# Kernel tuning notes

Hardware: AMD Instinct MI355X
Metric: run time of the kernel (lower is better)

Reference implementation:

```python
import jax, jax.numpy as jnp
import numpy as np

NUM_HEADS = 16
MAX_REL = 512  # max_relative_positions k


def setup_inputs() -> dict:
    key = jax.random.key(0)
    ks = jax.random.split(key, 8)
    B, S, H = 4, 1024, 1024
    R = 2 * MAX_REL + 1
    s = 0.02
    return {
        "hidden_states": jax.random.normal(ks[0], (B, S, H), jnp.float32),
        "attention_mask": jnp.zeros((B, 1, 1, S), jnp.float32),
        "rel_embeddings": jax.random.normal(ks[1], (R, H), jnp.float32),
        "Wq": jax.random.normal(ks[2], (H, H), jnp.float32) * s,
        "bq": jnp.zeros((H,), jnp.float32),
        "Wk": jax.random.normal(ks[3], (H, H), jnp.float32) * s,
        "bk": jnp.zeros((H,), jnp.float32),
        "Wv": jax.random.normal(ks[4], (H, H), jnp.float32) * s,
        "bv": jnp.zeros((H,), jnp.float32),
        "Wpk": jax.random.normal(ks[5], (H, H), jnp.float32) * s,
        "bpk": jnp.zeros((H,), jnp.float32),
        "Wpq": jax.random.normal(ks[6], (H, H), jnp.float32) * s,
        "bpq": jnp.zeros((H,), jnp.float32),
    }


def _heads(x, B, S):
    # [B,S,H] -> [B,nH,S,hd]
    return x.reshape(B, S, NUM_HEADS, -1).transpose(0, 2, 1, 3)


def reference(hidden_states, attention_mask, rel_embeddings,
              Wq, bq, Wk, bk, Wv, bv, Wpk, bpk, Wpq, bpq):
    B, S, H = hidden_states.shape
    hd = H // NUM_HEADS
    scale = 1.0 / np.sqrt(3.0 * hd).astype(np.float32)

    q = _heads(hidden_states @ Wq + bq, B, S)  # [B,nH,S,hd]
    k = _heads(hidden_states @ Wk + bk, B, S)
    v = _heads(hidden_states @ Wv + bv, B, S)

    # relative position bucket indices in [0, 2k]
    ids = jnp.arange(S)
    rel_pos = jnp.clip(ids[:, None] - ids[None, :], -MAX_REL, MAX_REL) + MAX_REL  # [S,S]

    rel_k = (rel_embeddings @ Wpk + bpk).reshape(-1, NUM_HEADS, hd)  # [R,nH,hd]
    rel_q = (rel_embeddings @ Wpq + bpq).reshape(-1, NUM_HEADS, hd)

    # 1) content-to-content
    c2c = jnp.einsum('bnih,bnjh->bnij', q, k)

    # 2) content-to-position: gather q.rel_k over rel bucket per (i,j)
    c2p_all = jnp.einsum('bnih,rnh->bnir', q, rel_k)  # [B,nH,S,R]
    idx = jnp.broadcast_to(rel_pos[None, None], (B, NUM_HEADS, S, S))
    c2p = jnp.take_along_axis(c2p_all, idx, axis=3)  # [B,nH,S,S]

    # 3) position-to-content: p2c[b,n,i,j] = (k_j . rel_q)[rel_pos[j,i]]
    p2c_all = jnp.einsum('bnjh,rnh->bnjr', k, rel_q)  # [B,nH,S,R]
    p2c_ji = jnp.take_along_axis(p2c_all, idx, axis=3)  # [B,nH,j,i]
    p2c = p2c_ji.transpose(0, 1, 3, 2)

    scores = (c2c + c2p + p2c) * scale + attention_mask
    probs = jax.nn.softmax(scores, axis=-1)
    ctx = jnp.einsum('bnij,bnjh->bnih', probs, v)
    ctx = ctx.transpose(0, 2, 1, 3).reshape(B, S, H)
    return ctx
```

## Files before the change

kernel.cpp:

```cpp
#include <hip/hip_runtime.h>
#include <stdint.h>

typedef unsigned short u16;
typedef __bf16 bf16_t;
typedef bf16_t bf16x8 __attribute__((ext_vector_type(8)));
typedef float f32x4 __attribute__((ext_vector_type(4)));

__device__ __forceinline__ u16 f2bf(float f) {
  union { float f; unsigned int u; } v; v.f = f;
  return (u16)((v.u + 0x7FFFu + ((v.u >> 16) & 1u)) >> 16);
}
__device__ __forceinline__ float bf2f(u16 b) {
  union { unsigned int u; float f; } v; v.u = ((unsigned int)b) << 16;
  return v.f;
}
__device__ __forceinline__ unsigned pk2bf(float a, float b) {
  return (unsigned)f2bf(a) | ((unsigned)f2bf(b) << 16);
}

#define MFMA16(a, b, c) __builtin_amdgcn_mfma_f32_16x16x32_bf16((a), (b), (c), 0, 0, 0)
#define GLL16(g, l) __builtin_amdgcn_global_load_lds( \
    (const __attribute__((address_space(1))) void*)(g), \
    (__attribute__((address_space(3))) void*)(l), 16, 0, 0)

#define SWZ(row, col) ((col) ^ (((row) & 7) << 3))

#define SCALE 0.07216878364870323f
#define SCALE_L2E 0.10411754546752362f
#define LOG2E 1.4426950408889634f
#define M8L2E -11.541560327111707f

__global__ void cvt_bf16(const float* __restrict__ in, u16* __restrict__ out, int n4) {
  int i = blockIdx.x * 256 + threadIdx.x;
  if (i >= n4) return;
  float4 v = ((const float4*)in)[i];
  ushort4 o;
  o.x = f2bf(v.x); o.y = f2bf(v.y); o.z = f2bf(v.z); o.w = f2bf(v.w);
  ((ushort4*)out)[i] = o;
}

__global__ void transp5_bf16(const float* __restrict__ i0, const float* __restrict__ i1,
                             const float* __restrict__ i2, const float* __restrict__ i3,
                             const float* __restrict__ i4,
                             u16* __restrict__ o0, u16* __restrict__ o1,
                             u16* __restrict__ o2, u16* __restrict__ o3,
                             u16* __restrict__ o4) {
  __shared__ float t[32][33];
  const float* in;
  u16* out;
  switch (blockIdx.z) {
    case 0: in = i0; out = o0; break;
    case 1: in = i1; out = o1; break;
    case 2: in = i2; out = o2; break;
    case 3: in = i3; out = o3; break;
    default: in = i4; out = o4; break;
  }
  int tx = threadIdx.x & 31, ty = threadIdx.x >> 5;
  int x0 = blockIdx.x * 32, y0 = blockIdx.y * 32;
  #pragma unroll
  for (int i = ty; i < 32; i += 8)
    t[i][tx] = in[(size_t)(y0 + i) * 1024 + x0 + tx];
  __syncthreads();
  #pragma unroll
  for (int i = ty; i < 32; i += 8)
    out[(size_t)(x0 + i) * 1024 + y0 + tx] = f2bf(t[tx][i]);
}

__global__ void __launch_bounds__(256) gemm_multi(
    const u16* __restrict__ A, const u16* __restrict__ BT,
    const float* __restrict__ b0, const float* __restrict__ b1, const float* __restrict__ b2,
    u16* __restrict__ out, int M, int rel) {
  __shared__ __align__(16) u16 As[4096];
  __shared__ __align__(16) u16 Bs[4096];
  const int K = 1024;
  const int mat = blockIdx.y >> 3;
  const u16* BTm = BT + (size_t)mat * 1048576;
  const float* bias = (mat == 0) ? b0 : ((mat == 1) ? b1 : b2);
  const int m0 = blockIdx.x * 128, n0 = (blockIdx.y & 7) * 128;
  const int w = threadIdx.x >> 6, lane = threadIdx.x & 63;
  const int lj = lane & 15, lg = lane >> 4;
  const int wm = (w >> 1) * 64, wn = (w & 1) * 64;

  f32x4 acc[4][4] = {};

  const int chunk0 = w * 128 + lane;
  const int chunk1 = chunk0 + 64;
  int r0 = chunk0 >> 2, s0 = (chunk0 & 3) * 8;
  int r1 = chunk1 >> 2, s1 = (chunk1 & 3) * 8;
  int ar0 = m0 + r0; if (ar0 >= M) ar0 = M - 1;
  int ar1 = m0 + r1; if (ar1 >= M) ar1 = M - 1;
  const u16* ga0 = A + (size_t)ar0 * K + s0;
  const u16* ga1 = A + (size_t)ar1 * K + s1;
  const u16* gb0 = BTm + (size_t)(n0 + r0) * K + s0;
  const u16* gb1 = BTm + (size_t)(n0 + r1) * K + s1;
  u16* lA0 = As + (w * 2 + 0) * 512;
  u16* lA1 = As + (w * 2 + 1) * 512;
  u16* lB0 = Bs + (w * 2 + 0) * 512;
  u16* lB1 = Bs + (w * 2 + 1) * 512;

  for (int k0 = 0; k0 < K; k0 += 32) {
    GLL16(ga0 + k0, lA0);
    GLL16(ga1 + k0, lA1);
    GLL16(gb0 + k0, lB0);
    GLL16(gb1 + k0, lB1);
    __syncthreads();
    bf16x8 af[4], bf8[4];
    #pragma unroll
    for (int mf = 0; mf < 4; ++mf)
      af[mf] = *(const bf16x8*)(As + (wm + mf * 16 + lj) * 32 + lg * 8);
    #pragma unroll
    for (int nf = 0; nf < 4; ++nf)
      bf8[nf] = *(const bf16x8*)(Bs + (wn + nf * 16 + lj) * 32 + lg * 8);
    #pragma unroll
    for (int mf = 0; mf < 4; ++mf)
      #pragma unroll
      for (int nf = 0; nf < 4; ++nf)
        acc[mf][nf] = MFMA16(af[mf], bf8[nf], acc[mf][nf]);
    __syncthreads();
  }

  #pragma unroll
  for (int mf = 0; mf < 4; ++mf) {
    #pragma unroll
    for (int nf = 0; nf < 4; ++nf) {
      const int j = n0 + wn + nf * 16 + lj;
      const float bj = bias[j];
      #pragma unroll
      for (int r = 0; r < 4; ++r) {
        const int i = m0 + wm + mf * 16 + lg * 4 + r;
        if (i >= M) continue;
        const u16 val = f2bf(acc[mf][nf][r] + bj);
        if (rel) {
          out[(size_t)mat * 1049600 + (size_t)(j >> 6) * 65600 + (size_t)i * 64 + (j & 63)] = val;
        } else if (mat < 2) {
          out[(size_t)mat * 4194304 +
              (size_t)(((i >> 10) << 4) + (j >> 6)) * 65536 + (size_t)(i & 1023) * 64 + (j & 63)] = val;
        } else {
          out[(size_t)2 * 4194304 +
              (size_t)(((i >> 10) << 4) + (j >> 6)) * 65536 + (size_t)(j & 63) * 1024 + (i & 1023)] = val;
        }
      }
    }
  }
}

__global__ void __launch_bounds__(256, 2) attn_fused(
    const u16* __restrict__ qg, const u16* __restrict__ kg, const u16* __restrict__ vtg,
    const u16* __restrict__ rkg, const u16* __restrict__ rqg,
    const float* __restrict__ mask, float* __restrict__ out) {
  __shared__ __align__(16) u16 Ks[64][64];
  __shared__ __align__(16) u16 Ps[64][64];
  __shared__ __align__(16) u16 RKs[128][64];
  __shared__ __align__(16) u16 RQs[128][64];
  __shared__ __align__(16) u16 Ts[64][128];
  __shared__ __align__(16) u16 Us[64][128];

  const int bx = ((blockIdx.x & 7) << 7) | (blockIdx.x >> 3);
  const int it = bx & 15, bn = bx >> 4;
  const int b = bn >> 4, n = bn & 15;
  const int i0 = it * 64;
  const int tid = threadIdx.x, w = tid >> 6, lane = tid & 63;
  const int lj = lane & 15, lg = lane >> 4;

  const u16* qh = qg + (size_t)bn * 65536;
  const u16* kh = kg + (size_t)bn * 65536;
  const u16* vth = vtg + (size_t)bn * 65536;
  const u16* rkh = rkg + (size_t)n * 65600;
  const u16* rqh = rqg + (size_t)n * 65600;
  const float* mk = mask + (size_t)b * 1024;

  const int l8 = lane >> 3, gK = (lane & 7) ^ l8;
  const u16* kb0  = kh  + (size_t)((w * 2 + 0) * 8 + l8) * 64 + gK * 8;
  const u16* kb1  = kh  + (size_t)((w * 2 + 1) * 8 + l8) * 64 + gK * 8;
  const u16* rkb0 = rkh + (size_t)((w * 4 + 0) * 8 + l8) * 64 + gK * 8;
  const u16* rkb1 = rkh + (size_t)((w * 4 + 1) * 8 + l8) * 64 + gK * 8;
  const u16* rkb2 = rkh + (size_t)((w * 4 + 2) * 8 + l8) * 64 + gK * 8;
  const u16* rkb3 = rkh + (size_t)((w * 4 + 3) * 8 + l8) * 64 + gK * 8;
  const u16* rqb0 = rqh + (size_t)((w * 4 + 0) * 8 + l8) * 64 + gK * 8;
  const u16* rqb1 = rqh + (size_t)((w * 4 + 1) * 8 + l8) * 64 + gK * 8;
  const u16* rqb2 = rqh + (size_t)((w * 4 + 2) * 8 + l8) * 64 + gK * 8;
  const u16* rqb3 = rqh + (size_t)((w * 4 + 3) * 8 + l8) * 64 + gK * 8;
  u16* ksd0 = &Ks[0][0]  + (w * 2 + 0) * 512;
  u16* ksd1 = &Ks[0][0]  + (w * 2 + 1) * 512;
  u16* rkd0 = &RKs[0][0] + (w * 4 + 0) * 512;
  u16* rkd1 = &RKs[0][0] + (w * 4 + 1) * 512;
  u16* rkd2 = &RKs[0][0] + (w * 4 + 2) * 512;
  u16* rkd3 = &RKs[0][0] + (w * 4 + 3) * 512;
  u16* rqd0 = &RQs[0][0] + (w * 4 + 0) * 512;
  u16* rqd1 = &RQs[0][0] + (w * 4 + 1) * 512;
  u16* rqd2 = &RQs[0][0] + (w * 4 + 2) * 512;
  u16* rqd3 = &RQs[0][0] + (w * 4 + 3) * 512;

#define STAGE_TILE(J0N) do { \
    const int ddn_ = i0 - (J0N) + 512; \
    int w0n_ = ddn_ - 63; w0n_ = w0n_ < 0 ? 0 : (w0n_ > 897 ? 897 : w0n_); \
    int w0qn_ = (1024 - ddn_) - 63; w0qn_ = w0qn_ < 0 ? 0 : (w0qn_ > 897 ? 897 : w0qn_); \
    GLL16(kb0 + (size_t)(J0N) * 64, ksd0); \
    GLL16(kb1 + (size_t)(J0N) * 64, ksd1); \
    GLL16(rkb0 + (size_t)w0n_ * 64, rkd0); \
    GLL16(rkb1 + (size_t)w0n_ * 64, rkd1); \
    GLL16(rkb2 + (size_t)w0n_ * 64, rkd2); \
    GLL16(rkb3 + (size_t)w0n_ * 64, rkd3); \
    GLL16(rqb0 + (size_t)w0qn_ * 64, rqd0); \
    GLL16(rqb1 + (size_t)w0qn_ * 64, rqd1); \
    GLL16(rqb2 + (size_t)w0qn_ * 64, rqd2); \
    GLL16(rqb3 + (size_t)w0qn_ * 64, rqd3); \
  } while (0)

  bf16x8 aq_all[4][2];
  #pragma unroll
  for (int f = 0; f < 4; ++f)
    #pragma unroll
    for (int k2 = 0; k2 < 2; ++k2)
      aq_all[f][k2] = *(const bf16x8*)(qh + (size_t)(i0 + f * 16 + lj) * 64 + k2 * 32 + lg * 8);
  bf16x8 aq_own[2];
  #pragma unroll
  for (int k2 = 0; k2 < 2; ++k2)
    aq_own[k2] = *(const bf16x8*)(qh + (size_t)(i0 + w * 16 + lj) * 64 + k2 * 32 + lg * 8);

  const u16* vrow[4];
  #pragma unroll
  for (int d = 0; d < 4; ++d)
    vrow[d] = vth + (size_t)(d * 16 + lj) * 1024 + lg * 8;

  const int swlj = (lj & 7) << 3;
  int baseT[4], swi[4], baseP[4];
  #pragma unroll
  for (int r = 0; r < 4; ++r) {
    const int il = w * 16 + lg * 4 + r;
    baseT[r] = il * 128;
    swi[r] = (il & 7) << 3;
    baseP[r] = il * 64;
  }
  const u16* Ts_f = &Ts[0][0];
  const u16* Us_f = &Us[0][0];
  u16* Ts_w = &Ts[0][0];
  u16* Us_w = &Us[0][0];
  u16* Ps_f = &Ps[0][0];

  float lsum[4] = {0.f, 0.f, 0.f, 0.f};
  f32x4 accO[4] = {};

  STAGE_TILE(0);

  for (int jt = 0; jt < 16; ++jt) {
    const int j0 = jt * 64;
    const int dd = i0 - j0 + 512;
    int w0 = dd - 63; w0 = w0 < 0 ? 0 : (w0 > 897 ? 897 : w0);
    int w0q = (1024 - dd) - 63; w0q = w0q < 0 ? 0 : (w0q > 897 ? 897 : w0q);

    __syncthreads();

    bf16x8 bk_all[4][2];
    #pragma unroll
    for (int f = 0; f < 4; ++f)
      #pragma unroll
      for (int k2 = 0; k2 < 2; ++k2) {
        const int kr = f * 16 + lj;
        bk_all[f][k2] = *(const bf16x8*)(&Ks[kr][SWZ(kr, k2 * 32 + lg * 8)]);
      }
    __builtin_amdgcn_s_setprio(1);
    f32x4 scc[4];
    #pragma unroll
    for (int jf = 0; jf < 4; ++jf) {
      scc[jf] = (f32x4){0.f, 0.f, 0.f, 0.f};
      #pragma unroll
      for (int k2 = 0; k2 < 2; ++k2)
        scc[jf] = MFMA16(aq_own[k2], bk_all[jf][k2], scc[jf]);
    }
    #pragma unroll
    for (int c16 = 0; c16 < 2; ++c16) {
      const int tc = w * 2 + c16;
      const int rr = tc * 16 + lj;
      bf16x8 brk[2], brq[2];
      #pragma unroll
      for (int k2 = 0; k2 < 2; ++k2) {
        brk[k2] = *(const bf16x8*)(&RKs[rr][SWZ(rr, k2 * 32 + lg * 8)]);
        brq[k2] = *(const bf16x8*)(&RQs[rr][SWZ(rr, k2 * 32 + lg * 8)]);
      }
      const int cb = (tc * 16 + lg * 4) ^ swlj;
      #pragma unroll
      for (int f = 0; f < 4; ++f) {
        f32x4 t_ = {0.f, 0.f, 0.f, 0.f};
        f32x4 u_ = {0.f, 0.f, 0.f, 0.f};
        #pragma unroll
        for (int k2 = 0; k2 < 2; ++k2) {
          t_ = MFMA16(brk[k2], aq_all[f][k2], t_);
          u_ = MFMA16(brq[k2], bk_all[f][k2], u_);
        }
        uint2 tp, up;
        tp.x = pk2bf(t_[0], t_[1]); tp.y = pk2bf(t_[2], t_[3]);
        up.x = pk2bf(u_[0], u_[1]); up.y = pk2bf(u_[2], u_[3]);
        *(uint2*)(Ts_w + (f * 16 + lj) * 128 + cb) = tp;
        *(uint2*)(Us_w + (f * 16 + lj) * 128 + cb) = up;
      }
    }
    __builtin_amdgcn_s_setprio(0);
    __syncthreads();

    if (jt < 15) STAGE_TILE(j0 + 64);

    bf16x8 vreg[8];
    #pragma unroll
    for (int jk = 0; jk < 2; ++jk)
      #pragma unroll
      for (int d = 0; d < 4; ++d)
        vreg[jk * 4 + d] = *(const bf16x8*)(vrow[d] + j0 + jk * 32);

    const int E = dd + w * 16 + lg * 4 - lj;
    const int C2 = 1024 - w0q;
    float mjs[4];
    #pragma unroll
    for (int jf = 0; jf < 4; ++jf)
      mjs[jf] = fmaf(mk[j0 + jf * 16 + lj], LOG2E, M8L2E);
    if (dd >= 63 && dd <= 961) {
      #pragma unroll
      for (int jf = 0; jf < 4; ++jf) {
        const int ubase = (jf * 16 + lj) * 128;
        #pragma unroll
        for (int r = 0; r < 4; ++r) {
          const int x1 = E + r - jf * 16;
          const float tT = bf2f(Ts_f[baseT[r] + ((x1 - w0) ^ swi[r])]);
          const float tU = bf2f(Us_f[ubase + ((C2 - x1) ^ swlj)]);
          const float p = __builtin_amdgcn_exp2f(
              fmaf(scc[jf][r] + tT + tU, SCALE_L2E, mjs[jf]));
          lsum[r] += p;
          Ps_f[baseP[r] + ((jf * 16 + lj) ^ (swi[r] & 56))] = f2bf(p);
        }
      }
    } else {
      #pragma unroll
      for (int jf = 0; jf < 4; ++jf) {
        const int ubase = (jf * 16 + lj) * 128;
        #pragma unroll
        for (int r = 0; r < 4; ++r) {
          int x1 = E + r - jf * 16;
          x1 = x1 < 0 ? 0 : (x1 > 1024 ? 1024 : x1);
          const float tT = bf2f(Ts_f[baseT[r] + ((x1 - w0) ^ swi[r])]);
          const float tU = bf2f(Us_f[ubase + ((C2 - x1) ^ swlj)]);
          const float p = __builtin_amdgcn_exp2f(
              fmaf(scc[jf][r] + tT + tU, SCALE_L2E, mjs[jf]));
          lsum[r] += p;
          Ps_f[baseP[r] + ((jf * 16 + lj) ^ (swi[r] & 56))] = f2bf(p);
        }
      }
    }
    __builtin_amdgcn_s_setprio(1);
    #pragma unroll
    for (int jk = 0; jk < 2; ++jk) {
      const int pr = w * 16 + lj;
      bf16x8 ap = *(const bf16x8*)(&Ps[pr][SWZ(pr, jk * 32 + lg * 8)]);
      #pragma unroll
      for (int d = 0; d < 4; ++d)
        accO[d] = MFMA16(ap, vreg[jk * 4 + d], accO[d]);
    }
    __builtin_amdgcn_s_setprio(0);
  }

  #pragma unroll
  for (int off = 1; off < 16; off <<= 1)
    #pragma unroll
    for (int r = 0; r < 4; ++r)
      lsum[r] += __shfl_xor(lsum[r], off);

  #pragma unroll
  for (int r = 0; r < 4; ++r) {
    const float inv = 1.f / lsum[r];
    const int i = i0 + w * 16 + lg * 4 + r;
    #pragma unroll
    for (int d = 0; d < 4; ++d)
      out[((size_t)b * 1024 + i) * 1024 + n * 64 + d * 16 + lj] = accO[d][r] * inv;
  }
#undef STAGE_TILE
}

extern "C" void kernel_launch(void* const* d_in, const int* in_sizes, int n_in,
                              void* d_out, int out_size, void* d_ws, size_t ws_size,
                              hipStream_t stream) {
  const float* hs   = (const float*)d_in[0];
  const float* mask = (const float*)d_in[1];
  const float* rel  = (const float*)d_in[2];
  const float* Wq   = (const float*)d_in[3];
  const float* bq   = (const float*)d_in[4];
  const float* Wk   = (const float*)d_in[5];
  const float* bk   = (const float*)d_in[6];
  const float* Wv   = (const float*)d_in[7];
  const float* bv   = (const float*)d_in[8];
  const float* Wpk  = (const float*)d_in[9];
  const float* bpk  = (const float*)d_in[10];
  const float* Wpq  = (const float*)d_in[11];
  const float* bpq  = (const float*)d_in[12];
  float* outp = (float*)d_out;

  u16* p = (u16*)d_ws;
  u16* hsb  = p; p += (size_t)4096 * 1024;
  u16* relb = p; p += (size_t)1025 * 1024;
  u16* WqT  = p; p += (size_t)1024 * 1024;
  u16* WkT  = p; p += (size_t)1024 * 1024;
  u16* WvT  = p; p += (size_t)1024 * 1024;
  u16* WpkT = p; p += (size_t)1024 * 1024;
  u16* WpqT = p; p += (size_t)1024 * 1024;
  u16* qws  = p; p += (size_t)4096 * 1024;
  u16* kws  = p; p += (size_t)4096 * 1024;
  u16* vws  = p; p += (size_t)4096 * 1024;
  u16* rkws = p; p += (size_t)16 * 1025 * 64;
  u16* rqws = p; p += (size_t)16 * 1025 * 64;
  if ((size_t)((char*)p - (char*)d_ws) > ws_size) return;
  (void)kws; (void)rqws;

  cvt_bf16<<<4096, 256, 0, stream>>>(hs, hsb, 1048576);
  cvt_bf16<<<1025, 256, 0, stream>>>(rel, relb, 262400);
  transp5_bf16<<<dim3(32, 32, 5), 256, 0, stream>>>(Wq, Wk, Wv, Wpk, Wpq,
                                                    WqT, WkT, WvT, WpkT, WpqT);

  gemm_multi<<<dim3(32, 24), 256, 0, stream>>>(hsb, WqT, bq, bk, bv, qws, 4096, 0);
  gemm_multi<<<dim3(9, 16),  256, 0, stream>>>(relb, WpkT, bpk, bpq, bpq, rkws, 1025, 1);

  attn_fused<<<1024, 256, 0, stream>>>(qws, kws, vws, rkws, rqws, mask, outp);
}
```

Before: 212.0 us.

## Merge prep kernels and give QKV GEMM a K=64 tile with swizzled grid

Folds the two fp32-to-bf16 conversion launches and the weight transpose launch into one prep kernel. The QKV projection gets its own GEMM with a 64-wide K tile, XOR-swizzled LDS layout and a block-index swizzle for L2 locality. The next tile's global-to-LDS load is issued after fragments are read into registers, so it overlaps the MFMAs. This cuts launch overhead and barrier count per K step, at the cost of more registers and larger LDS tiles.

```diff
diff --git a/kernel.cpp b/kernel.cpp
--- a/kernel.cpp
+++ b/kernel.cpp
@@ -30,33 +30,40 @@
 #define LOG2E 1.4426950408889634f
 #define M8L2E -11.541560327111707f
 
-__global__ void cvt_bf16(const float* __restrict__ in, u16* __restrict__ out, int n4) {
-  int i = blockIdx.x * 256 + threadIdx.x;
-  if (i >= n4) return;
-  float4 v = ((const float4*)in)[i];
-  ushort4 o;
-  o.x = f2bf(v.x); o.y = f2bf(v.y); o.z = f2bf(v.z); o.w = f2bf(v.w);
-  ((ushort4*)out)[i] = o;
-}
-
-__global__ void transp5_bf16(const float* __restrict__ i0, const float* __restrict__ i1,
-                             const float* __restrict__ i2, const float* __restrict__ i3,
-                             const float* __restrict__ i4,
-                             u16* __restrict__ o0, u16* __restrict__ o1,
-                             u16* __restrict__ o2, u16* __restrict__ o3,
-                             u16* __restrict__ o4) {
+__global__ void prep(const float* __restrict__ hs, const float* __restrict__ rel,
+                     const float* __restrict__ Wq, const float* __restrict__ Wk,
+                     const float* __restrict__ Wv, const float* __restrict__ Wpk,
+                     const float* __restrict__ Wpq,
+                     u16* __restrict__ hsb, u16* __restrict__ relb,
+                     u16* __restrict__ WqT, u16* __restrict__ WkT, u16* __restrict__ WvT,
+                     u16* __restrict__ WpkT, u16* __restrict__ WpqT) {
   __shared__ float t[32][33];
+  const int bid = blockIdx.x, tid = threadIdx.x;
+  if (bid < 5121) {
+    const float* in;
+    u16* out;
+    int i;
+    if (bid < 4096) { in = hs; out = hsb; i = bid * 256 + tid; }
+    else            { in = rel; out = relb; i = (bid - 4096) * 256 + tid; }
+    float4 v = ((const float4*)in)[i];
+    ushort4 o;
+    o.x = f2bf(v.x); o.y = f2bf(v.y); o.z = f2bf(v.z); o.w = f2bf(v.w);
+    ((ushort4*)out)[i] = o;
+    return;
+  }
+  const int tt = bid - 5121;
+  const int z = tt >> 10, rem = tt & 1023;
+  const int x0 = (rem & 31) * 32, y0 = (rem >> 5) * 32;
   const float* in;
   u16* out;
-  switch (blockIdx.z) {
-    case 0: in = i0; out = o0; break;
-    case 1: in = i1; out = o1; break;
-    case 2: in = i2; out = o2; break;
-    case 3: in = i3; out = o3; break;
-    default: in = i4; out = o4; break;
-  }
-  int tx = threadIdx.x & 31, ty = threadIdx.x >> 5;
-  int x0 = blockIdx.x * 32, y0 = blockIdx.y * 32;
+  switch (z) {
+    case 0: in = Wq; out = WqT; break;
+    case 1: in = Wk; out = WkT; break;
+    case 2: in = Wv; out = WvT; break;
+    case 3: in = Wpk; out = WpkT; break;
+    default: in = Wpq; out = WpqT; break;
+  }
+  int tx = tid & 31, ty = tid >> 5;
   #pragma unroll
   for (int i = ty; i < 32; i += 8)
     t[i][tx] = in[(size_t)(y0 + i) * 1024 + x0 + tx];
@@ -66,16 +73,106 @@
     out[(size_t)(x0 + i) * 1024 + y0 + tx] = f2bf(t[tx][i]);
 }
 
-__global__ void __launch_bounds__(256) gemm_multi(
+__global__ void __launch_bounds__(256) gemm_qkv(
     const u16* __restrict__ A, const u16* __restrict__ BT,
     const float* __restrict__ b0, const float* __restrict__ b1, const float* __restrict__ b2,
-    u16* __restrict__ out, int M, int rel) {
+    u16* __restrict__ out) {
+  __shared__ __align__(16) u16 As[128 * 64];
+  __shared__ __align__(16) u16 Bs[128 * 64];
+  const int K = 1024;
+  const int fid = blockIdx.y * 32 + blockIdx.x;
+  const int swz = (fid & 7) * 96 + (fid >> 3);
+  const int bxg = swz & 31, byg = swz >> 5;
+  const int mat = byg >> 3;
+  const u16* BTm = BT + (size_t)mat * 1048576;
+  const float* bias = (mat == 0) ? b0 : ((mat == 1) ? b1 : b2);
+  const int m0 = bxg * 128, n0 = (byg & 7) * 128;
+  const int w = threadIdx.x >> 6, lane = threadIdx.x & 63;
+  const int lj = lane & 15, lg = lane >> 4;
+  const int wm = (w >> 1) * 64, wn = (w & 1) * 64;
+  const int l8 = lane >> 3, gs = ((lane & 7) ^ l8) * 8;
+
+  f32x4 acc[4][4] = {};
+
+  const u16* ga[4]; const u16* gb[4];
+  u16* la[4]; u16* lb[4];
+  #pragma unroll
+  for (int c4 = 0; c4 < 4; ++c4) {
+    const int c = w * 4 + c4;
+    ga[c4] = A   + (size_t)(m0 + c * 8 + l8) * K + gs;
+    gb[c4] = BTm + (size_t)(n0 + c * 8 + l8) * K + gs;
+    la[c4] = As + c * 512;
+    lb[c4] = Bs + c * 512;
+  }
+  #pragma unroll
+  for (int c4 = 0; c4 < 4; ++c4) { GLL16(ga[c4], la[c4]); GLL16(gb[c4], lb[c4]); }
+
+  for (int k0 = 0; k0 < K; k0 += 64) {
+    __syncthreads();
+    bf16x8 af[2][4], bf[2][4];
+    #pragma unroll
+    for (int k2 = 0; k2 < 2; ++k2)
+      #pragma unroll
+      for (int mf = 0; mf < 4; ++mf) {
+        const int row = wm + mf * 16 + lj;
+        af[k2][mf] = *(const bf16x8*)(As + row * 64 + ((k2 * 4 + lg) ^ (row & 7)) * 8);
+      }
+    #pragma unroll
+    for (int k2 = 0; k2 < 2; ++k2)
+      #pragma unroll
+      for (int nf = 0; nf < 4; ++nf) {
+        const int row = wn + nf * 16 + lj;
+        bf[k2][nf] = *(const bf16x8*)(Bs + row * 64 + ((k2 * 4 + lg) ^ (row & 7)) * 8);
+      }
+    __syncthreads();
+    if (k0 + 64 < K) {
+      #pragma unroll
+      for (int c4 = 0; c4 < 4; ++c4) {
+        GLL16(ga[c4] + k0 + 64, la[c4]);
+        GLL16(gb[c4] + k0 + 64, lb[c4]);
+      }
+    }
+    #pragma unroll
+    for (int k2 = 0; k2 < 2; ++k2)
+      #pragma unroll
+      for (int mf = 0; mf < 4; ++mf)
+        #pragma unroll
+        for (int nf = 0; nf < 4; ++nf)
+          acc[mf][nf] = MFMA16(af[k2][mf], bf[k2][nf], acc[mf][nf]);
+  }
+
+  #pragma unroll
+  for (int mf = 0; mf < 4; ++mf) {
+    #pragma unroll
+    for (int nf = 0; nf < 4; ++nf) {
+      const int j = n0 + wn + nf * 16 + lj;
+      const float bj = bias[j];
+      #pragma unroll
+      for (int r = 0; r < 4; ++r) {
+        const int i = m0 + wm + mf * 16 + lg * 4 + r;
+        const u16 val = f2bf(acc[mf][nf][r] + bj);
+        if (mat < 2) {
+          out[(size_t)mat * 4194304 +
+              (size_t)(((i >> 10) << 4) + (j >> 6)) * 65536 + (size_t)(i & 1023) * 64 + (j & 63)] = val;
+        } else {
+          out[(size_t)2 * 4194304 +
+              (size_t)(((i >> 10) << 4) + (j >> 6)) * 65536 + (size_t)(j & 63) * 1024 + (i & 1023)] = val;
+        }
+      }
+    }
+  }
+}
+
+__global__ void __launch_bounds__(256) gemm_rel(
+    const u16* __restrict__ A, const u16* __restrict__ BT,
+    const float* __restrict__ b0, const float* __restrict__ b1,
+    u16* __restrict__ out, int M) {
   __shared__ __align__(16) u16 As[4096];
   __shared__ __align__(16) u16 Bs[4096];
   const int K = 1024;
   const int mat = blockIdx.y >> 3;
   const u16* BTm = BT + (size_t)mat * 1048576;
-  const float* bias = (mat == 0) ? b0 : ((mat == 1) ? b1 : b2);
+  const float* bias = (mat == 0) ? b0 : b1;
   const int m0 = blockIdx.x * 128, n0 = (blockIdx.y & 7) * 128;
   const int w = threadIdx.x >> 6, lane = threadIdx.x & 63;
   const int lj = lane & 15, lg = lane >> 4;
@@ -129,16 +226,8 @@
       for (int r = 0; r < 4; ++r) {
         const int i = m0 + wm + mf * 16 + lg * 4 + r;
         if (i >= M) continue;
-        const u16 val = f2bf(acc[mf][nf][r] + bj);
-        if (rel) {
-          out[(size_t)mat * 1049600 + (size_t)(j >> 6) * 65600 + (size_t)i * 64 + (j & 63)] = val;
-        } else if (mat < 2) {
-          out[(size_t)mat * 4194304 +
-              (size_t)(((i >> 10) << 4) + (j >> 6)) * 65536 + (size_t)(i & 1023) * 64 + (j & 63)] = val;
-        } else {
-          out[(size_t)2 * 4194304 +
-              (size_t)(((i >> 10) << 4) + (j >> 6)) * 65536 + (size_t)(j & 63) * 1024 + (i & 1023)] = val;
-        }
+        out[(size_t)mat * 1049600 + (size_t)(j >> 6) * 65600 + (size_t)i * 64 + (j & 63)] =
+            f2bf(acc[mf][nf][r] + bj);
       }
     }
   }
@@ -408,13 +497,9 @@
   if ((size_t)((char*)p - (char*)d_ws) > ws_size) return;
   (void)kws; (void)rqws;
 
-  cvt_bf16<<<4096, 256, 0, stream>>>(hs, hsb, 1048576);
-  cvt_bf16<<<1025, 256, 0, stream>>>(rel, relb, 262400);
-  transp5_bf16<<<dim3(32, 32, 5), 256, 0, stream>>>(Wq, Wk, Wv, Wpk, Wpq,
-                                                    WqT, WkT, WvT, WpkT, WpqT);
-
-  gemm_multi<<<dim3(32, 24), 256, 0, stream>>>(hsb, WqT, bq, bk, bv, qws, 4096, 0);
-  gemm_multi<<<dim3(9, 16),  256, 0, stream>>>(relb, WpkT, bpk, bpq, bpq, rkws, 1025, 1);
-
+  prep<<<10241, 256, 0, stream>>>(hs, rel, Wq, Wk, Wv, Wpk, Wpq,
+                                  hsb, relb, WqT, WkT, WvT, WpkT, WpqT);
+  gemm_qkv<<<dim3(32, 24), 256, 0, stream>>>(hsb, WqT, bq, bk, bv, qws);
+  gemm_rel<<<dim3(9, 16), 256, 0, stream>>>(relb, WpkT, bpk, bpq, rkws, 1025);
   attn_fused<<<1024, 256, 0, stream>>>(qws, kws, vws, rkws, rqws, mask, outp);
 }
```

Measured after the change: 217.4 us. 1.03x slower.
